# Kernel optimization log

Hardware: AMD Instinct MI355X
Metric: run time of the kernel (lower is better)

## Reference

```python
import jax, jax.numpy as jnp
import numpy as np

N_NODES = 50000
N_EDGES = 640000
IN_DIM = 5
HID = 128
NUM_GRAPHS = 512


def _graph_conv(x, src, dst, W_rel, b_rel, W_root):
    # PyG GraphConv (aggr='add'): out = lin_rel(sum_{j in N(i)} x_j) + lin_root(x_i)
    agg = jax.ops.segment_sum(x[src], dst, num_segments=N_NODES)  # [N, d_in]
    return agg @ W_rel + b_rel + x @ W_root


def setup_inputs() -> dict:
    key = jax.random.key(0)
    ks = jax.random.split(key, 16)
    x = jax.random.normal(ks[0], (N_NODES, IN_DIM), dtype=jnp.float32)
    edge_index = jax.random.randint(ks[1], (2, N_EDGES), 0, N_NODES, dtype=jnp.int32)
    batch = jnp.sort(jax.random.randint(ks[2], (N_NODES,), 0, NUM_GRAPHS, dtype=jnp.int32))

    def lin_w(k, fan_in, fan_out):
        bound = 1.0 / np.sqrt(fan_in)
        return jax.random.uniform(k, (fan_in, fan_out), jnp.float32, -bound, bound)

    def lin_b(k, fan_in, fan_out):
        bound = 1.0 / np.sqrt(fan_in)
        return jax.random.uniform(k, (fan_out,), jnp.float32, -bound, bound)

    params = {}
    dims = [(IN_DIM, HID), (HID, HID), (HID, HID)]
    for i, (di, do) in enumerate(dims):
        params[f"W_rel{i}"] = lin_w(ks[3 + 3 * i], di, do)
        params[f"b_rel{i}"] = lin_b(ks[4 + 3 * i], di, do)
        params[f"W_root{i}"] = lin_w(ks[5 + 3 * i], di, do)
    params["W_lin"] = lin_w(ks[12], HID, 1)
    params["b_lin"] = lin_b(ks[13], HID, 1)
    return {"x": x, "edge_index": edge_index, "batch": batch, **params}


def reference(x, edge_index, batch,
              W_rel0, b_rel0, W_root0,
              W_rel1, b_rel1, W_root1,
              W_rel2, b_rel2, W_root2,
              W_lin, b_lin):
    src, dst = edge_index[0], edge_index[1]
    # convs[:-1] with ReLU
    h = jax.nn.relu(_graph_conv(x, src, dst, W_rel0, b_rel0, W_root0))
    h = jax.nn.relu(_graph_conv(h, src, dst, W_rel1, b_rel1, W_root1))
    # last conv, no activation
    h = _graph_conv(h, src, dst, W_rel2, b_rel2, W_root2)
    # global_mean_pool over batch ids
    sums = jax.ops.segment_sum(h, batch, num_segments=NUM_GRAPHS)  # [G, HID]
    cnts = jax.ops.segment_sum(jnp.ones((h.shape[0],), h.dtype), batch, num_segments=NUM_GRAPHS)
    pooled = sums / jnp.maximum(cnts, 1.0)[:, None]
    # dropout(p=0.01) is identity in eval mode
    logits = pooled @ W_lin + b_lin  # [G, 1]
    return jax.nn.sigmoid(logits)
```

## Files before the change

### kernel.cpp

```cpp
#include <hip/hip_runtime.h>
#include <hip/hip_bf16.h>
#include <math.h>

#define N_NODES 50000
#define N_EDGES 640000
#define IN_DIM 5
#define HID 128
#define NGRAPH 512
#define BUCKET 64
#define GEMM_NBLK ((N_NODES + 63) / 64)
#define CNT_BLK ((N_EDGES + 255) / 256)
#define PREP_BLK 128
#define NROW_BLK ((N_NODES + 255) / 256)

typedef unsigned short u16;
typedef __attribute__((ext_vector_type(8))) short bf16x8;
typedef __attribute__((ext_vector_type(8))) unsigned short u16x8;
typedef __attribute__((ext_vector_type(4))) float f32x4;
typedef __attribute__((ext_vector_type(8))) float f32x8;

__device__ __forceinline__ float bf2f(u16 u) {
  union { unsigned int i; float f; } v; v.i = ((unsigned int)u) << 16; return v.f;
}
__device__ __forceinline__ u16 f2bf(float f) {
  return __bfloat16_as_ushort(__float2bfloat16(f));
}

__global__ __launch_bounds__(256) void setup_k(const int* __restrict__ src,
                                               const int* __restrict__ dst,
                                               int* __restrict__ cnt,
                                               int* __restrict__ slot,
                                               const float* __restrict__ W1rel,
                                               const float* __restrict__ W1root,
                                               u16* __restrict__ T1rel, u16* __restrict__ T1root,
                                               const float* __restrict__ Wrel2,
                                               const float* __restrict__ Wroot2,
                                               const float* __restrict__ b2,
                                               const float* __restrict__ Wlin,
                                               float* __restrict__ wvecs,
                                               const int* __restrict__ batch,
                                               int* __restrict__ nrow) {
  int b = blockIdx.x;
  if (b < CNT_BLK) {
    int e = b * 256 + threadIdx.x;
    if (e < N_EDGES) {
      int d = dst[e];
      int pos = atomicAdd(&cnt[d], 1);
      if (pos < BUCKET) slot[(size_t)d * BUCKET + pos] = src[e];
    }
  } else if (b < CNT_BLK + PREP_BLK) {
    int bb = b - CNT_BLK;
    int which = bb >> 6;
    int idx = (bb & 63) * 256 + threadIdx.x;
    const float* W = which == 0 ? W1rel : W1root;
    u16* T = which == 0 ? T1rel : T1root;
    int k = idx >> 7, n = idx & 127;
    T[n * HID + k] = f2bf(W[idx]);
  } else if (b == CNT_BLK + PREP_BLK) {
    int t = threadIdx.x;
    if (t < 128) {
      float s = 0.f;
      for (int c = 0; c < HID; ++c) s = fmaf(Wrel2[t * HID + c], Wlin[c], s);
      wvecs[t] = s;
    } else {
      int k = t - 128;
      float s = 0.f;
      for (int c = 0; c < HID; ++c) s = fmaf(Wroot2[k * HID + c], Wlin[c], s);
      wvecs[128 + k] = s;
    }
    if (t == 0) {
      float s = 0.f;
      for (int c = 0; c < HID; ++c) s = fmaf(b2[c], Wlin[c], s);
      wvecs[256] = s;
    }
  } else {
    int n = (b - CNT_BLK - PREP_BLK - 1) * 256 + threadIdx.x;
    if (n < N_NODES) {
      int bg = batch[n];
      int bp = (n == 0) ? -1 : batch[n - 1];
      for (int g = bp + 1; g <= bg; ++g) nrow[g] = n;
      if (n == N_NODES - 1) {
        for (int g = bg + 1; g <= NGRAPH; ++g) nrow[g] = N_NODES;
      }
    }
  }
}

__global__ __launch_bounds__(256) void agg5_k(const float* __restrict__ x,
                                              const int* __restrict__ cnt,
                                              const int* __restrict__ slot,
                                              float* __restrict__ A5) {
  int tid = threadIdx.x;
  int grp = tid >> 4;
  int l16 = tid & 15;
  int node = blockIdx.x * 16 + grp;
  if (node >= N_NODES) return;
  int deg = min(cnt[node], BUCKET);
  size_t base = (size_t)node * BUCKET;
  float a[IN_DIM];
#pragma unroll
  for (int k = 0; k < IN_DIM; ++k) a[k] = 0.f;
  for (int j = l16; j < deg; j += 16) {
    int s = slot[base + j];
#pragma unroll
    for (int k = 0; k < IN_DIM; ++k) a[k] += x[s * IN_DIM + k];
  }
#pragma unroll
  for (int k = 0; k < IN_DIM; ++k) {
    a[k] += __shfl_xor(a[k], 1, 16);
    a[k] += __shfl_xor(a[k], 2, 16);
    a[k] += __shfl_xor(a[k], 4, 16);
    a[k] += __shfl_xor(a[k], 8, 16);
  }
  if (l16 == 0) {
#pragma unroll
    for (int k = 0; k < IN_DIM; ++k) A5[node * IN_DIM + k] = a[k];
  }
}

__global__ __launch_bounds__(256, 3) void proj_gemm_k(const float* __restrict__ x,
                                                      const float* __restrict__ A5,
                                                      const float* __restrict__ Wrel0,
                                                      const float* __restrict__ Wroot0,
                                                      const float* __restrict__ brel0,
                                                      const u16* __restrict__ WrelT,
                                                      const u16* __restrict__ WrootT,
                                                      const float* __restrict__ bias1,
                                                      u16* __restrict__ Z,
                                                      u16* __restrict__ R) {
  __shared__ u16 As[64][136];
  const int tid = threadIdx.x;
  const int r0 = blockIdx.x * 64;

  {
    const int c0 = (tid & 63) * 2;
    const int rg = tid >> 6;
    float wr0[IN_DIM], wr1[IN_DIM], wo0[IN_DIM], wo1[IN_DIM];
#pragma unroll
    for (int k = 0; k < IN_DIM; ++k) {
      wr0[k] = Wrel0[k * HID + c0];
      wr1[k] = Wrel0[k * HID + c0 + 1];
      wo0[k] = Wroot0[k * HID + c0];
      wo1[k] = Wroot0[k * HID + c0 + 1];
    }
    const float b0 = brel0[c0], b1 = brel0[c0 + 1];
#pragma unroll
    for (int i = 0; i < 16; ++i) {
      int row = rg * 16 + i;
      int grow = r0 + row;
      float v0 = 0.f, v1 = 0.f;
      if (grow < N_NODES) {
        v0 = b0; v1 = b1;
#pragma unroll
        for (int k = 0; k < IN_DIM; ++k) {
          float a = A5[grow * IN_DIM + k];
          float xr = x[grow * IN_DIM + k];
          v0 = fmaf(a, wr0[k], fmaf(xr, wo0[k], v0));
          v1 = fmaf(a, wr1[k], fmaf(xr, wo1[k], v1));
        }
      }
      ushort2 w2;
      w2.x = f2bf(fmaxf(v0, 0.f));
      w2.y = f2bf(fmaxf(v1, 0.f));
      *(ushort2*)&As[row][c0] = w2;
    }
  }
  __syncthreads();

  const int wv = tid >> 6, lane = tid & 63;
  const int m = lane & 15, quad = lane >> 4;
  const u16* WT = (wv < 2) ? WrelT : WrootT;
  const int n0 = (wv & 1) * 64;

  f32x4 acc[4][4];
#pragma unroll
  for (int mt = 0; mt < 4; ++mt)
#pragma unroll
    for (int nt = 0; nt < 4; ++nt) acc[mt][nt] = (f32x4){0.f, 0.f, 0.f, 0.f};

#pragma unroll
  for (int ks = 0; ks < 4; ++ks) {
    int kb = ks * 32;
    bf16x8 af[4], bf[4];
#pragma unroll
    for (int mt = 0; mt < 4; ++mt)
      af[mt] = *(const bf16x8*)&As[mt * 16 + m][kb + quad * 8];
#pragma unroll
    for (int nt = 0; nt < 4; ++nt)
      bf[nt] = *(const bf16x8*)(WT + (size_t)(n0 + nt * 16 + m) * HID + kb + quad * 8);
#pragma unroll
    for (int mt = 0; mt < 4; ++mt)
#pragma unroll
      for (int nt = 0; nt < 4; ++nt)
        acc[mt][nt] = __builtin_amdgcn_mfma_f32_16x16x32_bf16(af[mt], bf[nt], acc[mt][nt], 0, 0, 0);
  }

  if (wv < 2) {
#pragma unroll
    for (int mt = 0; mt < 4; ++mt)
#pragma unroll
      for (int nt = 0; nt < 4; ++nt) {
        int col = n0 + nt * 16 + m;
#pragma unroll
        for (int r = 0; r < 4; ++r) {
          int row = r0 + mt * 16 + quad * 4 + r;
          if (row < N_NODES) Z[(size_t)row * HID + col] = f2bf(acc[mt][nt][r]);
        }
      }
  } else {
    float bl[4];
#pragma unroll
    for (int nt = 0; nt < 4; ++nt) bl[nt] = bias1[n0 + nt * 16 + m];
#pragma unroll
    for (int mt = 0; mt < 4; ++mt)
#pragma unroll
      for (int nt = 0; nt < 4; ++nt) {
        int col = n0 + nt * 16 + m;
#pragma unroll
        for (int r = 0; r < 4; ++r) {
          int row = r0 + mt * 16 + quad * 4 + r;
          if (row < N_NODES) R[(size_t)row * HID + col] = f2bf(acc[mt][nt][r] + bl[nt]);
        }
      }
  }
}

__device__ __forceinline__ void gather_node(const u16* __restrict__ Z,
                                            const int* __restrict__ esrc,
                                            int beg, int end, int q, int f8,
                                            f32x8& out) {
  f32x8 a0, a1;
#pragma unroll
  for (int j = 0; j < 8; ++j) { a0[j] = 0.f; a1[j] = 0.f; }
  int e = beg + q;
  for (; e + 4 < end; e += 8) {
    int s0 = esrc[e];
    int s1 = esrc[e + 4];
    u16x8 za = *(const u16x8*)(Z + (size_t)s0 * HID + f8);
    u16x8 zb = *(const u16x8*)(Z + (size_t)s1 * HID + f8);
#pragma unroll
    for (int j = 0; j < 8; ++j) { a0[j] += bf2f(za[j]); a1[j] += bf2f(zb[j]); }
  }
  if (e < end) {
    int s0 = esrc[e];
    u16x8 za = *(const u16x8*)(Z + (size_t)s0 * HID + f8);
#pragma unroll
    for (int j = 0; j < 8; ++j) a0[j] += bf2f(za[j]);
  }
#pragma unroll
  for (int j = 0; j < 8; ++j) out[j] = a0[j] + a1[j];
}

__global__ __launch_bounds__(256) void agg_s_k(const u16* __restrict__ Z,
                                               const int* __restrict__ cnt,
                                               const int* __restrict__ slot,
                                               const u16* __restrict__ R,
                                               const float* __restrict__ wvecs,
                                               float* __restrict__ s_rel,
                                               float* __restrict__ s_root) {
  int wave = threadIdx.x >> 6;
  int lane = threadIdx.x & 63;
  int node = blockIdx.x * 4 + wave;
  if (node >= N_NODES) return;
  int q = lane >> 4;
  int l16 = lane & 15;
  int f8 = l16 * 8;
  int beg = node * BUCKET;
  int end = beg + min(cnt[node], BUCKET);
  f32x8 acc;
  gather_node(Z, slot, beg, end, q, f8, acc);
#pragma unroll
  for (int j = 0; j < 8; ++j) {
    acc[j] += __shfl_xor(acc[j], 16, 64);
    acc[j] += __shfl_xor(acc[j], 32, 64);
  }
  if (q == 0) {
    const u16* rp = R + (size_t)node * HID + f8;
    u16x8 r8 = *(const u16x8*)rp;
    float sr = 0.f, so = 0.f;
#pragma unroll
    for (int j = 0; j < 8; ++j) {
      float h = fmaxf(bf2f(r8[j]) + acc[j], 0.f);
      sr = fmaf(h, wvecs[f8 + j], sr);
      so = fmaf(h, wvecs[128 + f8 + j], so);
    }
#pragma unroll
    for (int w = 1; w < 16; w <<= 1) {
      sr += __shfl_xor(sr, w, 16);
      so += __shfl_xor(so, w, 16);
    }
    if (l16 == 0) {
      s_rel[node] = sr;
      s_root[node] = so;
    }
  }
}

__global__ __launch_bounds__(256) void pool_final_k(const float* __restrict__ s_rel,
                                                    const float* __restrict__ s_root,
                                                    const int* __restrict__ cnt,
                                                    const int* __restrict__ slot,
                                                    const int* __restrict__ nrow,
                                                    const float* __restrict__ wvecs,
                                                    const float* __restrict__ blin,
                                                    float* __restrict__ out) {
  int g = blockIdx.x;
  int n0 = nrow[g], n1 = nrow[g + 1];
  int wave = threadIdx.x >> 6;
  int lane = threadIdx.x & 63;
  float s = 0.f;
  for (int n = n0 + wave; n < n1; n += 4) {
    int deg = min(cnt[n], BUCKET);
    if (lane < deg) s += s_rel[slot[(size_t)n * BUCKET + lane]];
  }
  for (int n = n0 + threadIdx.x; n < n1; n += 256) s += s_root[n];
  __shared__ float red[4];
#pragma unroll
  for (int w = 32; w; w >>= 1) s += __shfl_down(s, w, 64);
  if (lane == 0) red[wave] = s;
  __syncthreads();
  if (threadIdx.x == 0) {
    float t = red[0] + red[1] + red[2] + red[3];
    float cntf = (float)(n1 - n0);
    float cmax = fmaxf(cntf, 1.f);
    float logit = (t + cntf * wvecs[256]) / cmax + blin[0];
    out[g] = 1.f / (1.f + expf(-logit));
  }
}


extern "C" void kernel_launch(void* const* d_in, const int* in_sizes, int n_in,
                              void* d_out, int out_size, void* d_ws, size_t ws_size,
                              hipStream_t stream) {
  const float* x      = (const float*)d_in[0];
  const int*   ei     = (const int*)d_in[1];
  const int*   batch  = (const int*)d_in[2];
  const float* Wrel0  = (const float*)d_in[3];
  const float* brel0  = (const float*)d_in[4];
  const float* Wroot0 = (const float*)d_in[5];
  const float* Wrel1  = (const float*)d_in[6];
  const float* brel1  = (const float*)d_in[7];
  const float* Wroot1 = (const float*)d_in[8];
  const float* Wrel2  = (const float*)d_in[9];
  const float* brel2  = (const float*)d_in[10];
  const float* Wroot2 = (const float*)d_in[11];
  const float* Wlin   = (const float*)d_in[12];
  const float* blin   = (const float*)d_in[13];
  float* out = (float*)d_out;
  const int* srcp = ei;
  const int* dstp = ei + N_EDGES;

  char* ws = (char*)d_ws;
  size_t off = 0;
  auto alloc = [&](size_t b) { size_t o = off; off += (b + 255) & ~(size_t)255; return (void*)(ws + o); };
  u16*  Z      = (u16*)alloc(sizeof(u16) * N_NODES * HID);
  u16*  R      = (u16*)alloc(sizeof(u16) * N_NODES * HID);
  float* s_rel  = (float*)alloc(sizeof(float) * N_NODES);
  float* s_root = (float*)alloc(sizeof(float) * N_NODES);
  u16* WT1rel  = (u16*)alloc(sizeof(u16) * HID * HID);
  u16* WT1root = (u16*)alloc(sizeof(u16) * HID * HID);
  float* wvecs = (float*)alloc(sizeof(float) * 260);
  int* nrow    = (int*)alloc(sizeof(int) * (NGRAPH + 1));
  int* slot    = (int*)alloc(sizeof(int) * (size_t)N_NODES * BUCKET);
  float* A5    = (float*)alloc(sizeof(float) * (size_t)N_NODES * IN_DIM);
  size_t zero_base = off;
  int*   cnt  = (int*)alloc(sizeof(int) * N_NODES);
  size_t zero_len = off - zero_base;

  hipMemsetAsync(ws + zero_base, 0, zero_len, stream);

  setup_k<<<CNT_BLK + PREP_BLK + 1 + NROW_BLK, 256, 0, stream>>>(
      srcp, dstp, cnt, slot, Wrel1, Wroot1, WT1rel, WT1root,
      Wrel2, Wroot2, brel2, Wlin, wvecs, batch, nrow);
  agg5_k<<<(N_NODES + 15) / 16, 256, 0, stream>>>(x, cnt, slot, A5);
  proj_gemm_k<<<GEMM_NBLK, 256, 0, stream>>>(x, A5, Wrel0, Wroot0, brel0,
                                             WT1rel, WT1root, brel1, Z, R);
  agg_s_k<<<(N_NODES + 3) / 4, 256, 0, stream>>>(Z, cnt, slot, R, wvecs, s_rel, s_root);
  pool_final_k<<<NGRAPH, 256, 0, stream>>>(s_rel, s_root, cnt, slot, nrow, wvecs, blin, out);
}
```

Measured before the change: 201.5 us.

## Fuse layer-0 aggregation into projection GEMM and vectorize setup edge pass

Removes the separate agg5 kernel and computes the 5-dim neighbor sums inside proj_gemm_k, with four threads per node and the results held in shared memory. This drops one launch and the A5 global round trip. Setup now has each thread handle four edges through int4 loads, and the weight-transpose prep uses float4 loads with fewer blocks. In exchange, gather latency is added at the start of every GEMM block, with only four lanes per node.

```diff
diff --git a/kernel.cpp b/kernel.cpp
--- a/kernel.cpp
+++ b/kernel.cpp
@@ -9,8 +9,8 @@
 #define NGRAPH 512
 #define BUCKET 64
 #define GEMM_NBLK ((N_NODES + 63) / 64)
-#define CNT_BLK ((N_EDGES + 255) / 256)
-#define PREP_BLK 128
+#define EDGE_BLK (N_EDGES / 1024)
+#define TPREP_BLK 32
 #define NROW_BLK ((N_NODES + 255) / 256)
 
 typedef unsigned short u16;
@@ -41,22 +41,30 @@
                                                const int* __restrict__ batch,
                                                int* __restrict__ nrow) {
   int b = blockIdx.x;
-  if (b < CNT_BLK) {
-    int e = b * 256 + threadIdx.x;
-    if (e < N_EDGES) {
-      int d = dst[e];
-      int pos = atomicAdd(&cnt[d], 1);
-      if (pos < BUCKET) slot[(size_t)d * BUCKET + pos] = src[e];
-    }
-  } else if (b < CNT_BLK + PREP_BLK) {
-    int bb = b - CNT_BLK;
-    int which = bb >> 6;
-    int idx = (bb & 63) * 256 + threadIdx.x;
+  if (b < EDGE_BLK) {
+    int e0 = (b * 256 + threadIdx.x) * 4;
+    int4 s4 = *(const int4*)(src + e0);
+    int4 d4 = *(const int4*)(dst + e0);
+    int ss[4] = {s4.x, s4.y, s4.z, s4.w};
+    int dd[4] = {d4.x, d4.y, d4.z, d4.w};
+#pragma unroll
+    for (int j = 0; j < 4; ++j) {
+      int pos = atomicAdd(&cnt[dd[j]], 1);
+      if (pos < BUCKET) slot[(size_t)dd[j] * BUCKET + pos] = ss[j];
+    }
+  } else if (b < EDGE_BLK + TPREP_BLK) {
+    int idx4 = ((b - EDGE_BLK) * 256 + threadIdx.x) * 4;
+    int which = idx4 >> 14;
+    int i = idx4 & (HID * HID - 1);
     const float* W = which == 0 ? W1rel : W1root;
     u16* T = which == 0 ? T1rel : T1root;
-    int k = idx >> 7, n = idx & 127;
-    T[n * HID + k] = f2bf(W[idx]);
-  } else if (b == CNT_BLK + PREP_BLK) {
+    int k = i >> 7, n = i & 127;
+    float4 w4 = *(const float4*)(W + i);
+    T[(n + 0) * HID + k] = f2bf(w4.x);
+    T[(n + 1) * HID + k] = f2bf(w4.y);
+    T[(n + 2) * HID + k] = f2bf(w4.z);
+    T[(n + 3) * HID + k] = f2bf(w4.w);
+  } else if (b == EDGE_BLK + TPREP_BLK) {
     int t = threadIdx.x;
     if (t < 128) {
       float s = 0.f;
@@ -74,7 +82,7 @@
       wvecs[256] = s;
     }
   } else {
-    int n = (b - CNT_BLK - PREP_BLK - 1) * 256 + threadIdx.x;
+    int n = (b - EDGE_BLK - TPREP_BLK - 1) * 256 + threadIdx.x;
     if (n < N_NODES) {
       int bg = batch[n];
       int bp = (n == 0) ? -1 : batch[n - 1];
@@ -86,40 +94,9 @@
   }
 }
 
-__global__ __launch_bounds__(256) void agg5_k(const float* __restrict__ x,
-                                              const int* __restrict__ cnt,
-                                              const int* __restrict__ slot,
-                                              float* __restrict__ A5) {
-  int tid = threadIdx.x;
-  int grp = tid >> 4;
-  int l16 = tid & 15;
-  int node = blockIdx.x * 16 + grp;
-  if (node >= N_NODES) return;
-  int deg = min(cnt[node], BUCKET);
-  size_t base = (size_t)node * BUCKET;
-  float a[IN_DIM];
-#pragma unroll
-  for (int k = 0; k < IN_DIM; ++k) a[k] = 0.f;
-  for (int j = l16; j < deg; j += 16) {
-    int s = slot[base + j];
-#pragma unroll
-    for (int k = 0; k < IN_DIM; ++k) a[k] += x[s * IN_DIM + k];
-  }
-#pragma unroll
-  for (int k = 0; k < IN_DIM; ++k) {
-    a[k] += __shfl_xor(a[k], 1, 16);
-    a[k] += __shfl_xor(a[k], 2, 16);
-    a[k] += __shfl_xor(a[k], 4, 16);
-    a[k] += __shfl_xor(a[k], 8, 16);
-  }
-  if (l16 == 0) {
-#pragma unroll
-    for (int k = 0; k < IN_DIM; ++k) A5[node * IN_DIM + k] = a[k];
-  }
-}
-
 __global__ __launch_bounds__(256, 3) void proj_gemm_k(const float* __restrict__ x,
-                                                      const float* __restrict__ A5,
+                                                      const int* __restrict__ cnt,
+                                                      const int* __restrict__ slot,
                                                       const float* __restrict__ Wrel0,
                                                       const float* __restrict__ Wroot0,
                                                       const float* __restrict__ brel0,
@@ -129,8 +106,37 @@
                                                       u16* __restrict__ Z,
                                                       u16* __restrict__ R) {
   __shared__ u16 As[64][136];
+  __shared__ float A5s[64][IN_DIM];
   const int tid = threadIdx.x;
   const int r0 = blockIdx.x * 64;
+
+  {
+    const int li = tid >> 2;
+    const int l4 = tid & 3;
+    const int node = r0 + li;
+    float a[IN_DIM];
+#pragma unroll
+    for (int k = 0; k < IN_DIM; ++k) a[k] = 0.f;
+    if (node < N_NODES) {
+      int deg = min(cnt[node], BUCKET);
+      size_t base = (size_t)node * BUCKET;
+      for (int j = l4; j < deg; j += 4) {
+        int s = slot[base + j];
+#pragma unroll
+        for (int k = 0; k < IN_DIM; ++k) a[k] += x[s * IN_DIM + k];
+      }
+    }
+#pragma unroll
+    for (int k = 0; k < IN_DIM; ++k) {
+      a[k] += __shfl_xor(a[k], 1, 64);
+      a[k] += __shfl_xor(a[k], 2, 64);
+    }
+    if (l4 == 0) {
+#pragma unroll
+      for (int k = 0; k < IN_DIM; ++k) A5s[li][k] = a[k];
+    }
+  }
+  __syncthreads();
 
   {
     const int c0 = (tid & 63) * 2;
@@ -153,7 +159,7 @@
         v0 = b0; v1 = b1;
 #pragma unroll
         for (int k = 0; k < IN_DIM; ++k) {
-          float a = A5[grow * IN_DIM + k];
+          float a = A5s[row][k];
           float xr = x[grow * IN_DIM + k];
           v0 = fmaf(a, wr0[k], fmaf(xr, wo0[k], v0));
           v1 = fmaf(a, wr1[k], fmaf(xr, wo1[k], v1));
@@ -362,18 +368,16 @@
   float* wvecs = (float*)alloc(sizeof(float) * 260);
   int* nrow    = (int*)alloc(sizeof(int) * (NGRAPH + 1));
   int* slot    = (int*)alloc(sizeof(int) * (size_t)N_NODES * BUCKET);
-  float* A5    = (float*)alloc(sizeof(float) * (size_t)N_NODES * IN_DIM);
   size_t zero_base = off;
   int*   cnt  = (int*)alloc(sizeof(int) * N_NODES);
   size_t zero_len = off - zero_base;
 
   hipMemsetAsync(ws + zero_base, 0, zero_len, stream);
 
-  setup_k<<<CNT_BLK + PREP_BLK + 1 + NROW_BLK, 256, 0, stream>>>(
+  setup_k<<<EDGE_BLK + TPREP_BLK + 1 + NROW_BLK, 256, 0, stream>>>(
       srcp, dstp, cnt, slot, Wrel1, Wroot1, WT1rel, WT1root,
       Wrel2, Wroot2, brel2, Wlin, wvecs, batch, nrow);
-  agg5_k<<<(N_NODES + 15) / 16, 256, 0, stream>>>(x, cnt, slot, A5);
-  proj_gemm_k<<<GEMM_NBLK, 256, 0, stream>>>(x, A5, Wrel0, Wroot0, brel0,
+  proj_gemm_k<<<GEMM_NBLK, 256, 0, stream>>>(x, cnt, slot, Wrel0, Wroot0, brel0,
                                              WT1rel, WT1root, brel1, Z, R);
   agg_s_k<<<(N_NODES + 3) / 4, 256, 0, stream>>>(Z, cnt, slot, R, wvecs, s_rel, s_root);
   pool_final_k<<<NGRAPH, 256, 0, stream>>>(s_rel, s_root, cnt, slot, nrow, wvecs, blin, out);
```

Result: no change. 200.4 us (-0.6%).
